# Optimization experiments

Hardware: AMD Instinct MI355X
Metric: run time of the kernel (lower is better)

## Reference

```python
import jax, jax.numpy as jnp
import numpy as np

BOARD_CELLS = 16  # 4x4 board, flattened
NUM_VALS = 16     # tile exponents 0..15


def _symmetries(pattern):
    """Replicates NTupleApproximator.generate_symmetries: 4 rotations x 2 reflections,
    each symmetry returned as the SORTED list of flat indices (matches the
    'i for i in range(16) if flat[i]==1' construction in the original)."""
    a = np.zeros(BOARD_CELLS)
    a[pattern] = 1
    a = a.reshape(4, 4)
    syms = []
    for _ in range(2):
        for _ in range(4):
            syms.append(np.flatnonzero(a.flatten() == 1).tolist())
            a = np.rot90(a)
        a = a.T
    return syms


def setup_inputs() -> dict:
    key = jax.random.key(0)
    k1, k2 = jax.random.split(key)
    patterns = [[0, 1, 2, 3, 4, 5], [4, 5, 6, 7, 8, 9],
                [0, 1, 2, 4, 5, 6], [4, 5, 6, 8, 9, 10]]
    sym, tid = [], []
    for pi, p in enumerate(patterns):
        for s in _symmetries(p):
            sym.append(s)
            tid.append(pi)  # == pi_sym // 8 in the original
    sym_coords = jnp.asarray(np.array(sym, dtype=np.int32))   # [32, 6]
    table_ids = jnp.asarray(np.array(tid, dtype=np.int32))    # [32]
    B = 65536
    # boards hold tile exponents directly (tile_to_index output), 0..15
    boards = jax.random.randint(k1, (B, BOARD_CELLS), 0, NUM_VALS, dtype=jnp.int32)
    # 4 tables of 16^6 entries each (normally trained; random here)
    weights = jax.random.normal(k2, (len(patterns), NUM_VALS ** 6), dtype=jnp.float32) * 0.01
    return {"boards": boards, "weights": weights,
            "sym_coords": sym_coords, "table_ids": table_ids}


def reference(boards, weights, sym_coords, table_ids):
    # boards: [B,16] int32 tile exponents; sym_coords: [P,L]; table_ids: [P]
    L = sym_coords.shape[1]
    # feat = fold(feat*16 + x) over coords  ==  dot(tiles, 16^{L-1-j})
    powers = (NUM_VALS ** jnp.arange(L - 1, -1, -1)).astype(jnp.int32)  # [L]
    tiles = boards[:, sym_coords]                 # [B,P,L] gather of cells
    feats = jnp.sum(tiles * powers, axis=-1)      # [B,P] base-16 feature index
    vals = weights[table_ids[None, :], feats]     # [B,P] table gather
    return vals.sum(axis=1)                       # [B] board values
```

## Files before the change

### kernel.cpp

```cpp
#include <hip/hip_runtime.h>


static constexpr int NSYM = 32;
static constexpr int TLEN = 6;

__global__ __launch_bounds__(256) void ntuple_eval_kernel(
    const int* __restrict__ boards,
    const float* __restrict__ weights,
    const int* __restrict__ sym_coords,
    const int* __restrict__ table_ids,
    float* __restrict__ out, int B)
{
    __shared__ int s_coords[NSYM * TLEN];
    __shared__ int s_base[NSYM];

    const int t = threadIdx.x;
    if (t < NSYM * TLEN) s_coords[t] = sym_coords[t];
    if (t < NSYM)        s_base[t]   = table_ids[t] << 24;
    __syncthreads();

    const int b = blockIdx.x * blockDim.x + t;
    if (b >= B) return;

    const int4* bp = reinterpret_cast<const int4*>(boards + (size_t)b * 16);
    const int4 r0 = bp[0], r1 = bp[1], r2 = bp[2], r3 = bp[3];

    const int c[16] = {r0.x, r0.y, r0.z, r0.w,
                       r1.x, r1.y, r1.z, r1.w,
                       r2.x, r2.y, r2.z, r2.w,
                       r3.x, r3.y, r3.z, r3.w};
    unsigned long long packed = 0ull;
#pragma unroll
    for (int i = 0; i < 16; ++i)
        packed |= (unsigned long long)((unsigned)c[i] & 15u) << (4 * i);

    float acc = 0.0f;
#pragma unroll
    for (int s = 0; s < NSYM; ++s) {
        int feat = 0;
#pragma unroll
        for (int j = 0; j < TLEN; ++j) {
            const int cc = s_coords[s * TLEN + j];
            feat = (feat << 4) | (int)((packed >> (cc << 2)) & 15ull);
        }
        acc += weights[(size_t)(s_base[s] + feat)];
    }
    out[b] = acc;
}

extern "C" void kernel_launch(void* const* d_in, const int* in_sizes, int n_in,
                              void* d_out, int out_size, void* d_ws, size_t ws_size,
                              hipStream_t stream) {
    const int*   boards     = (const int*)d_in[0];
    const float* weights    = (const float*)d_in[1];
    const int*   sym_coords = (const int*)d_in[2];
    const int*   table_ids  = (const int*)d_in[3];
    float*       out        = (float*)d_out;

    const int B = in_sizes[0] / 16;
    const int block = 256;
    const int grid = (B + block - 1) / block;
    ntuple_eval_kernel<<<grid, block, 0, stream>>>(boards, weights, sym_coords,
                                                   table_ids, out, B);
}
```

Measured before the change: 339.4 us.

## Bucket table lookups by weight tile and stream tiles through LDS

After: 473.3 us. +39.5%, slower.

```diff
diff --git a/kernel.cpp b/kernel.cpp
--- a/kernel.cpp
+++ b/kernel.cpp
@@ -4,11 +4,20 @@
 static constexpr int NSYM = 32;
 static constexpr int TLEN = 6;
 
-__global__ __launch_bounds__(256) void ntuple_eval_kernel(
+static constexpr int TILE_LOG2 = 13;
+static constexpr int TILE      = 1 << TILE_LOG2;
+static constexpr int TOTAL_ENTRIES_LOG2 = 26;
+static constexpr int NBUCKETS  = 1 << (TOTAL_ENTRIES_LOG2 - TILE_LOG2);
+static constexpr int CAP       = 512;
+
+
+__global__ __launch_bounds__(256) void phaseA_bucket(
     const int* __restrict__ boards,
     const float* __restrict__ weights,
     const int* __restrict__ sym_coords,
     const int* __restrict__ table_ids,
+    unsigned int* __restrict__ cnt,
+    unsigned int* __restrict__ recs,
     float* __restrict__ out, int B)
 {
     __shared__ int s_coords[NSYM * TLEN];
@@ -19,33 +28,65 @@
     if (t < NSYM)        s_base[t]   = table_ids[t] << 24;
     __syncthreads();
 
-    const int b = blockIdx.x * blockDim.x + t;
+    const int g = blockIdx.x * 256 + t;
+    const int b = g >> 3;
+    const int chunk = g & 7;
     if (b >= B) return;
 
     const int4* bp = reinterpret_cast<const int4*>(boards + (size_t)b * 16);
     const int4 r0 = bp[0], r1 = bp[1], r2 = bp[2], r3 = bp[3];
-
-    const int c[16] = {r0.x, r0.y, r0.z, r0.w,
-                       r1.x, r1.y, r1.z, r1.w,
-                       r2.x, r2.y, r2.z, r2.w,
-                       r3.x, r3.y, r3.z, r3.w};
+    const int c[16] = {r0.x, r0.y, r0.z, r0.w, r1.x, r1.y, r1.z, r1.w,
+                       r2.x, r2.y, r2.z, r2.w, r3.x, r3.y, r3.z, r3.w};
     unsigned long long packed = 0ull;
 #pragma unroll
     for (int i = 0; i < 16; ++i)
         packed |= (unsigned long long)((unsigned)c[i] & 15u) << (4 * i);
 
-    float acc = 0.0f;
 #pragma unroll
-    for (int s = 0; s < NSYM; ++s) {
+    for (int k = 0; k < 4; ++k) {
+        const int s = chunk * 4 + k;
         int feat = 0;
 #pragma unroll
         for (int j = 0; j < TLEN; ++j) {
             const int cc = s_coords[s * TLEN + j];
             feat = (feat << 4) | (int)((packed >> (cc << 2)) & 15ull);
         }
-        acc += weights[(size_t)(s_base[s] + feat)];
+        const unsigned flat = (unsigned)(s_base[s] + feat);
+        const unsigned bucket = flat >> TILE_LOG2;
+        const unsigned slot = atomicAdd(&cnt[bucket], 1u);
+        if (slot < CAP) {
+            recs[(size_t)bucket * CAP + slot] =
+                ((unsigned)b << TILE_LOG2) | (flat & (TILE - 1u));
+        } else {
+            atomicAdd(&out[b], weights[(size_t)flat]);
+        }
     }
-    out[b] = acc;
+}
+
+__global__ __launch_bounds__(256) void phaseB_stream(
+    const float* __restrict__ weights,
+    const unsigned int* __restrict__ cnt,
+    const unsigned int* __restrict__ recs,
+    float* __restrict__ out)
+{
+    __shared__ float tile[TILE];
+
+    const int bid = blockIdx.x;
+    const int t = threadIdx.x;
+
+    const float4* w4 = reinterpret_cast<const float4*>(weights + ((size_t)bid << TILE_LOG2));
+    float4* t4 = reinterpret_cast<float4*>(tile);
+#pragma unroll
+    for (int k = 0; k < TILE / 4 / 256; ++k)
+        t4[k * 256 + t] = w4[k * 256 + t];
+    __syncthreads();
+
+    unsigned n = cnt[bid];
+    if (n > CAP) n = CAP;
+    for (unsigned i = t; i < n; i += 256) {
+        const unsigned rec = recs[(size_t)bid * CAP + i];
+        atomicAdd(&out[rec >> TILE_LOG2], tile[rec & (TILE - 1u)]);
+    }
 }
 
 extern "C" void kernel_launch(void* const* d_in, const int* in_sizes, int n_in,
@@ -57,9 +98,17 @@
     const int*   table_ids  = (const int*)d_in[3];
     float*       out        = (float*)d_out;
 
+    unsigned int* cnt  = (unsigned int*)d_ws;
+    unsigned int* recs = cnt + NBUCKETS;
+
     const int B = in_sizes[0] / 16;
-    const int block = 256;
-    const int grid = (B + block - 1) / block;
-    ntuple_eval_kernel<<<grid, block, 0, stream>>>(boards, weights, sym_coords,
-                                                   table_ids, out, B);
+
+    hipMemsetAsync(out, 0, (size_t)out_size * sizeof(float), stream);
+    hipMemsetAsync(cnt, 0, (size_t)NBUCKETS * sizeof(unsigned int), stream);
+
+    const int totalA = B * 8;
+    phaseA_bucket<<<(totalA + 255) / 256, 256, 0, stream>>>(
+        boards, weights, sym_coords, table_ids, cnt, recs, out, B);
+
+    phaseB_stream<<<NBUCKETS, 256, 0, stream>>>(weights, cnt, recs, out);
 }
```

## Bucket-sort table lookups by weight region and serve buckets from LDS tiles

Applied to the files above, without the earlier changes.

Result: slower. 439.8 us (+29.6%).

```diff
diff --git a/kernel.cpp b/kernel.cpp
--- a/kernel.cpp
+++ b/kernel.cpp
@@ -3,48 +3,220 @@
 
 static constexpr int NSYM = 32;
 static constexpr int TLEN = 6;
-
-__global__ __launch_bounds__(256) void ntuple_eval_kernel(
-    const int* __restrict__ boards,
-    const float* __restrict__ weights,
-    const int* __restrict__ sym_coords,
-    const int* __restrict__ table_ids,
-    float* __restrict__ out, int B)
+static constexpr int BLOG = 13;
+static constexpr int NBUCK = 1 << (26 - BLOG);
+static constexpr int BMASK = (1 << BLOG) - 1;
+static constexpr int NA = 64;
+static constexpr int BPB = 1024;
+
+__device__ __forceinline__ unsigned long long pack_board(const int* boards, int b) {
+    const int4* bp = reinterpret_cast<const int4*>(boards + (size_t)b * 16);
+    const int4 r0 = bp[0], r1 = bp[1], r2 = bp[2], r3 = bp[3];
+    const int c[16] = {r0.x, r0.y, r0.z, r0.w, r1.x, r1.y, r1.z, r1.w,
+                       r2.x, r2.y, r2.z, r2.w, r3.x, r3.y, r3.z, r3.w};
+    unsigned long long p = 0ull;
+#pragma unroll
+    for (int i = 0; i < 16; ++i)
+        p |= (unsigned long long)((unsigned)c[i] & 15u) << (4 * i);
+    return p;
+}
+
+__device__ __forceinline__ unsigned feat_of(unsigned long long packed,
+                                            const int* s_coords, const int* s_base, int s) {
+    unsigned f = 0;
+#pragma unroll
+    for (int j = 0; j < TLEN; ++j) {
+        const int cc = s_coords[s * TLEN + j];
+        f = (f << 4) | (unsigned)((packed >> (cc << 2)) & 15ull);
+    }
+    return f + (unsigned)s_base[s];
+}
+
+__global__ __launch_bounds__(1024) void k1_hist(
+    const int* __restrict__ boards, const int* __restrict__ sym_coords,
+    const int* __restrict__ table_ids, unsigned* __restrict__ hist)
 {
     __shared__ int s_coords[NSYM * TLEN];
     __shared__ int s_base[NSYM];
-
+    __shared__ unsigned s_cnt[NBUCK];
     const int t = threadIdx.x;
     if (t < NSYM * TLEN) s_coords[t] = sym_coords[t];
     if (t < NSYM)        s_base[t]   = table_ids[t] << 24;
-    __syncthreads();
-
-    const int b = blockIdx.x * blockDim.x + t;
+#pragma unroll
+    for (int k = 0; k < NBUCK / 1024; ++k) s_cnt[k * 1024 + t] = 0u;
+    __syncthreads();
+
+    const int a = blockIdx.x;
+    const int b = a * BPB + t;
+    const unsigned long long packed = pack_board(boards, b);
+#pragma unroll
+    for (int s = 0; s < NSYM; ++s) {
+        const unsigned flat = feat_of(packed, s_coords, s_base, s);
+        atomicAdd(&s_cnt[flat >> BLOG], 1u);
+    }
+    __syncthreads();
+#pragma unroll
+    for (int k = 0; k < NBUCK / 1024; ++k)
+        hist[(size_t)a * NBUCK + k * 1024 + t] = s_cnt[k * 1024 + t];
+}
+
+__global__ __launch_bounds__(256) void k2_colprefix(
+    unsigned* __restrict__ hist, unsigned* __restrict__ tot)
+{
+    __shared__ unsigned T[64 * 65];
+    const int t = threadIdx.x;
+    const int j0 = blockIdx.x * 64;
+#pragma unroll
+    for (int r = 0; r < 16; ++r) {
+        const int idx = r * 256 + t;
+        const int a = idx >> 6, jj = idx & 63;
+        T[jj * 65 + a] = hist[(size_t)a * NBUCK + j0 + jj];
+    }
+    __syncthreads();
+    if (t < 64) {
+        unsigned run = 0;
+#pragma unroll
+        for (int a = 0; a < 64; ++a) {
+            const unsigned v = T[t * 65 + a];
+            T[t * 65 + a] = run;
+            run += v;
+        }
+        tot[j0 + t] = run;
+    }
+    __syncthreads();
+#pragma unroll
+    for (int r = 0; r < 16; ++r) {
+        const int idx = r * 256 + t;
+        const int a = idx >> 6, jj = idx & 63;
+        hist[(size_t)a * NBUCK + j0 + jj] = T[jj * 65 + a];
+    }
+}
+
+__global__ __launch_bounds__(256) void k3_scan(
+    const unsigned* __restrict__ tot, unsigned* __restrict__ base)
+{
+    __shared__ unsigned s_tot[NBUCK];
+    __shared__ unsigned s_w[4];
+    const int t = threadIdx.x;
+#pragma unroll
+    for (int k = 0; k < NBUCK / 256; ++k) s_tot[k * 256 + t] = tot[k * 256 + t];
+    __syncthreads();
+
+    unsigned lsum = 0;
+#pragma unroll
+    for (int k = 0; k < 32; ++k) lsum += s_tot[t * 32 + k];
+
+    unsigned v = lsum;
+    for (int d = 1; d < 64; d <<= 1) {
+        unsigned u = __shfl_up(v, d, 64);
+        if ((t & 63) >= d) v += u;
+    }
+    const int w = t >> 6;
+    if ((t & 63) == 63) s_w[w] = v;
+    __syncthreads();
+    unsigned woff = 0;
+    for (int k = 0; k < 4; ++k) if (k < w) woff += s_w[k];
+    unsigned run = v - lsum + woff;
+
+    for (int k = 0; k < 32; ++k) {
+        base[t * 32 + k] = run;
+        run += s_tot[t * 32 + k];
+    }
+    if (t == 255) base[NBUCK] = run;
+}
+
+__global__ __launch_bounds__(1024) void k4_scatter(
+    const int* __restrict__ boards, const int* __restrict__ sym_coords,
+    const int* __restrict__ table_ids, const unsigned* __restrict__ hist,
+    const unsigned* __restrict__ base, unsigned short* __restrict__ offs,
+    unsigned* __restrict__ pos_of)
+{
+    __shared__ int s_coords[NSYM * TLEN];
+    __shared__ int s_base[NSYM];
+    __shared__ unsigned s_cnt[NBUCK];
+    const int t = threadIdx.x;
+    if (t < NSYM * TLEN) s_coords[t] = sym_coords[t];
+    if (t < NSYM)        s_base[t]   = table_ids[t] << 24;
+#pragma unroll
+    for (int k = 0; k < NBUCK / 1024; ++k) s_cnt[k * 1024 + t] = 0u;
+    __syncthreads();
+
+    const int a = blockIdx.x;
+    const int b = a * BPB + t;
+    const unsigned long long packed = pack_board(boards, b);
+    const unsigned* hrow = hist + (size_t)a * NBUCK;
+    unsigned mypos[NSYM];
+#pragma unroll
+    for (int s = 0; s < NSYM; ++s) {
+        const unsigned flat = feat_of(packed, s_coords, s_base, s);
+        const unsigned j = flat >> BLOG;
+        const unsigned rank = atomicAdd(&s_cnt[j], 1u);
+        const unsigned pos = base[j] + hrow[j] + rank;
+        offs[pos] = (unsigned short)(flat & BMASK);
+        mypos[s] = pos;
+    }
+    unsigned* pp = pos_of + (size_t)b * NSYM;
+#pragma unroll
+    for (int s = 0; s < NSYM; ++s) pp[s] = mypos[s];
+}
+
+__global__ __launch_bounds__(256) void k5_serve(
+    const float* __restrict__ weights, const unsigned* __restrict__ base,
+    const unsigned short* __restrict__ offs, float* __restrict__ val)
+{
+    __shared__ float tile[1 << BLOG];
+    __shared__ unsigned s_rng[2];
+    const int j = blockIdx.x;
+    const int t = threadIdx.x;
+    const float4* w4 = reinterpret_cast<const float4*>(weights + ((size_t)j << BLOG));
+    float4* t4 = reinterpret_cast<float4*>(tile);
+#pragma unroll
+    for (int k = 0; k < (1 << BLOG) / 4 / 256; ++k)
+        t4[k * 256 + t] = w4[k * 256 + t];
+    if (t < 2) s_rng[t] = base[j + t];
+    __syncthreads();
+    const unsigned s0 = s_rng[0], s1 = s_rng[1];
+    for (unsigned i = s0 + t; i < s1; i += 256)
+        val[i] = tile[offs[i]];
+}
+
+__global__ __launch_bounds__(256) void k6_reduce(
+    const unsigned* __restrict__ pos_of, const float* __restrict__ val,
+    float* __restrict__ out, int B)
+{
+    const int b = blockIdx.x * 256 + threadIdx.x;
     if (b >= B) return;
-
-    const int4* bp = reinterpret_cast<const int4*>(boards + (size_t)b * 16);
-    const int4 r0 = bp[0], r1 = bp[1], r2 = bp[2], r3 = bp[3];
-
-    const int c[16] = {r0.x, r0.y, r0.z, r0.w,
-                       r1.x, r1.y, r1.z, r1.w,
-                       r2.x, r2.y, r2.z, r2.w,
-                       r3.x, r3.y, r3.z, r3.w};
-    unsigned long long packed = 0ull;
-#pragma unroll
-    for (int i = 0; i < 16; ++i)
-        packed |= (unsigned long long)((unsigned)c[i] & 15u) << (4 * i);
-
+    const uint4* pp = reinterpret_cast<const uint4*>(pos_of + (size_t)b * NSYM);
     float acc = 0.0f;
 #pragma unroll
-    for (int s = 0; s < NSYM; ++s) {
-        int feat = 0;
-#pragma unroll
-        for (int j = 0; j < TLEN; ++j) {
-            const int cc = s_coords[s * TLEN + j];
-            feat = (feat << 4) | (int)((packed >> (cc << 2)) & 15ull);
-        }
-        acc += weights[(size_t)(s_base[s] + feat)];
-    }
+    for (int k = 0; k < NSYM / 4; ++k) {
+        const uint4 p = pp[k];
+        acc += val[p.x];
+        acc += val[p.y];
+        acc += val[p.z];
+        acc += val[p.w];
+    }
+    out[b] = acc;
+}
+
+__global__ __launch_bounds__(256) void direct_kernel(
+    const int* __restrict__ boards, const float* __restrict__ weights,
+    const int* __restrict__ sym_coords, const int* __restrict__ table_ids,
+    float* __restrict__ out, int B)
+{
+    __shared__ int s_coords[NSYM * TLEN];
+    __shared__ int s_base[NSYM];
+    const int t = threadIdx.x;
+    if (t < NSYM * TLEN) s_coords[t] = sym_coords[t];
+    if (t < NSYM)        s_base[t]   = table_ids[t] << 24;
+    __syncthreads();
+    const int b = blockIdx.x * 256 + t;
+    if (b >= B) return;
+    const unsigned long long packed = pack_board(boards, b);
+    float acc = 0.0f;
+#pragma unroll
+    for (int s = 0; s < NSYM; ++s)
+        acc += weights[(size_t)feat_of(packed, s_coords, s_base, s)];
     out[b] = acc;
 }
 
@@ -56,10 +228,28 @@
     const int*   sym_coords = (const int*)d_in[2];
     const int*   table_ids  = (const int*)d_in[3];
     float*       out        = (float*)d_out;
-
     const int B = in_sizes[0] / 16;
-    const int block = 256;
-    const int grid = (B + block - 1) / block;
-    ntuple_eval_kernel<<<grid, block, 0, stream>>>(boards, weights, sym_coords,
-                                                   table_ids, out, B);
-}
+
+    if (B != NA * BPB) {
+        direct_kernel<<<(B + 255) / 256, 256, 0, stream>>>(
+            boards, weights, sym_coords, table_ids, out, B);
+        return;
+    }
+
+    const int NREC = B * NSYM;
+    char* w = (char*)d_ws;
+    unsigned*       hist   = (unsigned*)w;              w += (size_t)NA * NBUCK * 4;
+    unsigned*       tot    = (unsigned*)w;              w += (size_t)NBUCK * 4;
+    unsigned*       base   = (unsigned*)w;              w += (size_t)(NBUCK + 4) * 4;
+    unsigned short* offs   = (unsigned short*)w;        w += (size_t)NREC * 2;
+    unsigned*       pos_of = (unsigned*)w;              w += (size_t)NREC * 4;
+    float*          val    = (float*)w;
+
+    k1_hist   <<<NA,        1024, 0, stream>>>(boards, sym_coords, table_ids, hist);
+    k2_colprefix<<<NBUCK/64, 256, 0, stream>>>(hist, tot);
+    k3_scan   <<<1,          256, 0, stream>>>(tot, base);
+    k4_scatter<<<NA,        1024, 0, stream>>>(boards, sym_coords, table_ids,
+                                               hist, base, offs, pos_of);
+    k5_serve  <<<NBUCK,      256, 0, stream>>>(weights, base, offs, val);
+    k6_reduce <<<(B+255)/256,256, 0, stream>>>(pos_of, val, out, B);
+}
```
